# Kernel optimization log

Measured on AMD Instinct MI355X. Metric: run time of the kernel, lower is better.

## Reference

```python
import jax, jax.numpy as jnp
import numpy as np

DIM = 512
CROSS_DIM = 512
NUM_HEADS = 8
DIM_HEAD = 64
INNER = NUM_HEADS * DIM_HEAD  # 512
SCALE = DIM_HEAD ** -0.5


def setup_inputs() -> dict:
    key = jax.random.key(0)
    ks = jax.random.split(key, 7)
    B, S, C = 2, 4096, 4096
    x = jax.random.normal(ks[0], (B, S, DIM), dtype=jnp.float32)
    context = jax.random.normal(ks[1], (B, C, CROSS_DIM), dtype=jnp.float32)
    # nn.Linear weights stored as [out, in]; we apply x @ W.T
    w_q = jax.random.normal(ks[2], (INNER, DIM), dtype=jnp.float32) * (DIM ** -0.5)
    w_k = jax.random.normal(ks[3], (INNER, CROSS_DIM), dtype=jnp.float32) * (CROSS_DIM ** -0.5)
    w_v = jax.random.normal(ks[4], (INNER, CROSS_DIM), dtype=jnp.float32) * (CROSS_DIM ** -0.5)
    w_out = jax.random.normal(ks[5], (DIM, INNER), dtype=jnp.float32) * (INNER ** -0.5)
    b_out = jax.random.normal(ks[6], (DIM,), dtype=jnp.float32) * 0.02
    return {"x": x, "context": context, "w_q": w_q, "w_k": w_k,
            "w_v": w_v, "w_out": w_out, "b_out": b_out}


def reference(x, context, w_q, w_k, w_v, w_out, b_out):
    B, S, _ = x.shape
    _, C, _ = context.shape
    # projections -> [B, H, L, Dh]
    q = (x @ w_q.T).reshape(B, S, NUM_HEADS, DIM_HEAD).transpose(0, 2, 1, 3)
    k = (context @ w_k.T).reshape(B, C, NUM_HEADS, DIM_HEAD).transpose(0, 2, 1, 3)
    v = (context @ w_v.T).reshape(B, C, NUM_HEADS, DIM_HEAD).transpose(0, 2, 1, 3)
    # scores [B, H, S, C]
    scores = jnp.einsum('bhsd,bhcd->bhsc', q, k) * SCALE
    attn = jax.nn.softmax(scores, axis=-1)
    out = jnp.einsum('bhsc,bhcd->bhsd', attn, v)  # [B,H,S,Dh]
    out = out.transpose(0, 2, 1, 3).reshape(B, S, INNER)
    return out @ w_out.T + b_out
```

## Files before the change

### kernel.cpp

```cpp
#include <hip/hip_runtime.h>

typedef __bf16 bf16;
typedef __bf16 bf16x2 __attribute__((ext_vector_type(2)));
typedef __bf16 bf16x4 __attribute__((ext_vector_type(4)));
typedef __bf16 bf16x8 __attribute__((ext_vector_type(8)));
typedef float  f32x4  __attribute__((ext_vector_type(4)));
typedef float  f32x16 __attribute__((ext_vector_type(16)));
typedef unsigned int uint4v __attribute__((ext_vector_type(4)));

#define MFMA16(a,b,c) __builtin_amdgcn_mfma_f32_16x16x32_bf16(a,b,c,0,0,0)
#define MFMA32(a,b,c) __builtin_amdgcn_mfma_f32_32x32x16_bf16(a,b,c,0,0,0)

#if __has_builtin(__builtin_amdgcn_exp2f)
#define EXP2(x) __builtin_amdgcn_exp2f(x)
#else
#define EXP2(x) exp2f(x)
#endif

__device__ __forceinline__ void gl16(const bf16* __restrict__ g, bf16* l)
{
#if __has_builtin(__builtin_amdgcn_global_load_lds)
    __builtin_amdgcn_global_load_lds(
        (const __attribute__((address_space(1))) void*)g,
        (__attribute__((address_space(3))) void*)l, 16, 0, 0);
#else
    const int ln = __builtin_amdgcn_mbcnt_hi(~0u, __builtin_amdgcn_mbcnt_lo(~0u, 0));
    *(bf16x8*)((bf16*)l + ln * 8) = *(const bf16x8*)g;
#endif
}

__device__ __forceinline__ bf16x8 ld8_f32_to_bf16(const float* __restrict__ p)
{
    f32x4 a = *(const f32x4*)p;
    f32x4 b = *(const f32x4*)(p + 4);
    bf16x8 o;
#pragma unroll
    for (int j = 0; j < 4; j++) { o[j] = (bf16)a[j]; o[4 + j] = (bf16)b[j]; }
    return o;
}

__device__ __forceinline__ float max3f(float a, float b, float c)
{
    return fmaxf(fmaxf(a, b), c);
}

__device__ __forceinline__ float rmax16(const f32x16& s)
{
    const float a0 = max3f(s[0],  s[1],  s[2]);
    const float a1 = max3f(s[3],  s[4],  s[5]);
    const float a2 = max3f(s[6],  s[7],  s[8]);
    const float a3 = max3f(s[9],  s[10], s[11]);
    const float a4 = max3f(s[12], s[13], s[14]);
    return fmaxf(max3f(a0, a1, a2), max3f(a3, a4, s[15]));
}

__global__ __launch_bounds__(256) void cvt6(
    const float* __restrict__ x,  const float* __restrict__ ctx,
    const float* __restrict__ wq, const float* __restrict__ wk,
    const float* __restrict__ wv, const float* __restrict__ wout,
    bf16* __restrict__ xb, bf16* __restrict__ cb, bf16* __restrict__ wqb,
    bf16* __restrict__ wkb, bf16* __restrict__ wvb, bf16* __restrict__ wob)
{
    const int bid = blockIdx.x;
    const float* s; bf16* d; int base;
    if      (bid < 2048) { s = x;    d = xb;  base = 0;    }
    else if (bid < 4096) { s = ctx;  d = cb;  base = 2048; }
    else if (bid < 4224) { s = wq;   d = wqb; base = 4096; }
    else if (bid < 4352) { s = wk;   d = wkb; base = 4224; }
    else if (bid < 4480) { s = wv;   d = wvb; base = 4352; }
    else                 { s = wout; d = wob; base = 4480; }
    const int i = ((bid - base) * 256 + threadIdx.x) * 8;
    *(bf16x8*)&d[i] = ld8_f32_to_bf16(s + i);
}

__global__ __launch_bounds__(256, 3) void mm_qkv(
    const bf16* __restrict__ xb, const bf16* __restrict__ cb,
    const bf16* __restrict__ wqb, const bf16* __restrict__ wkb,
    const bf16* __restrict__ wvb,
    bf16* __restrict__ Qb, bf16* __restrict__ Kb, bf16* __restrict__ Vtb)
{
    __shared__ bf16 Al[128 * 32];
    __shared__ bf16 Wl[128 * 32];

    const int L  = blockIdx.x + 4 * (blockIdx.y + 64 * blockIdx.z);
    const int L2 = (L & 7) * 96 + (L >> 3);
    const int bx = L2 & 3;
    const int by = (L2 >> 2) & 63;
    const int z  = L2 >> 8;

    const bf16* A; const bf16* W; bf16* out; int mode;
    if (z == 0)      { A = xb; W = wqb; out = Qb;  mode = 0; }
    else if (z == 1) { A = cb; W = wkb; out = Kb;  mode = 0; }
    else             { A = cb; W = wvb; out = Vtb; mode = 1; }

    const int tid  = threadIdx.x;
    const int lane = tid & 63;
    const int w    = tid >> 6;
    const int wr   = w >> 1, wc = w & 1;
    const int q    = lane >> 4, m0 = lane & 15;

    f32x4 acc[4][4];
#pragma unroll
    for (int i = 0; i < 4; i++)
#pragma unroll
        for (int j = 0; j < 4; j++)
#pragma unroll
            for (int r = 0; r < 4; r++) acc[i][j][r] = 0.f;

    const bf16* Ab = A + (size_t)(by * 128) * 512;
    const bf16* Wb = W + (size_t)(bx * 128) * 512;
    const int sr = w * 16 + (lane >> 2);
    const int sc = (lane & 3) * 8;

    for (int k0 = 0; k0 < 512; k0 += 32) {
        gl16(Ab + (size_t)sr * 512 + k0 + sc,        &Al[(w * 16) * 32]);
        gl16(Ab + (size_t)(sr + 64) * 512 + k0 + sc, &Al[(64 + w * 16) * 32]);
        gl16(Wb + (size_t)sr * 512 + k0 + sc,        &Wl[(w * 16) * 32]);
        gl16(Wb + (size_t)(sr + 64) * 512 + k0 + sc, &Wl[(64 + w * 16) * 32]);
        __syncthreads();

        bf16x8 af[4], wf[4];
#pragma unroll
        for (int mt = 0; mt < 4; mt++)
            af[mt] = *(const bf16x8*)&Al[(wr * 64 + mt * 16 + m0) * 32 + q * 8];
#pragma unroll
        for (int nt = 0; nt < 4; nt++)
            wf[nt] = *(const bf16x8*)&Wl[(wc * 64 + nt * 16 + m0) * 32 + q * 8];
#pragma unroll
        for (int mt = 0; mt < 4; mt++)
#pragma unroll
            for (int nt = 0; nt < 4; nt++)
                acc[mt][nt] = MFMA16(af[mt], wf[nt], acc[mt][nt]);
        __syncthreads();
    }

#pragma unroll
    for (int nt = 0; nt < 4; nt++) {
        const int col = bx * 128 + wc * 64 + nt * 16 + m0;
#pragma unroll
        for (int mt = 0; mt < 4; mt++) {
            const int row0 = by * 128 + wr * 64 + mt * 16 + q * 4;
            if (mode == 0) {
#pragma unroll
                for (int r = 0; r < 4; r++)
                    out[(size_t)(row0 + r) * 512 + col] = (bf16)acc[mt][nt][r];
            } else {
                const int bb = row0 >> 12, c = row0 & 4095;
                const int hh = col >> 6,  d = col & 63;
                bf16x4 o4;
#pragma unroll
                for (int r = 0; r < 4; r++) o4[r] = (bf16)acc[mt][nt][r];
                *(bf16x4*)&out[(size_t)((bb * 8 + hh) * 64 + d) * 4096 + c] = o4;
            }
        }
    }
}

__global__ __launch_bounds__(256, 3) void mm_oproj(
    const bf16* __restrict__ Ob, const bf16* __restrict__ wob,
    const float* __restrict__ bout, float* __restrict__ out)
{
    __shared__ bf16 Al[128 * 32];
    __shared__ bf16 Wl[128 * 32];

    const int L  = blockIdx.x + 4 * blockIdx.y;
    const int L2 = (L & 7) * 32 + (L >> 3);
    const int bx = L2 & 3;
    const int by = L2 >> 2;

    const int tid  = threadIdx.x;
    const int lane = tid & 63;
    const int w    = tid >> 6;
    const int wr   = w >> 1, wc = w & 1;
    const int q    = lane >> 4, m0 = lane & 15;

    f32x4 acc[4][4];
#pragma unroll
    for (int i = 0; i < 4; i++)
#pragma unroll
        for (int j = 0; j < 4; j++)
#pragma unroll
            for (int r = 0; r < 4; r++) acc[i][j][r] = 0.f;

    const bf16* Ab = Ob  + (size_t)(by * 128) * 512;
    const bf16* Wb = wob + (size_t)(bx * 128) * 512;
    const int sr = w * 16 + (lane >> 2);
    const int sc = (lane & 3) * 8;

    for (int k0 = 0; k0 < 512; k0 += 32) {
        gl16(Ab + (size_t)sr * 512 + k0 + sc,        &Al[(w * 16) * 32]);
        gl16(Ab + (size_t)(sr + 64) * 512 + k0 + sc, &Al[(64 + w * 16) * 32]);
        gl16(Wb + (size_t)sr * 512 + k0 + sc,        &Wl[(w * 16) * 32]);
        gl16(Wb + (size_t)(sr + 64) * 512 + k0 + sc, &Wl[(64 + w * 16) * 32]);
        __syncthreads();

        bf16x8 af[4], wf[4];
#pragma unroll
        for (int mt = 0; mt < 4; mt++)
            af[mt] = *(const bf16x8*)&Al[(wr * 64 + mt * 16 + m0) * 32 + q * 8];
#pragma unroll
        for (int nt = 0; nt < 4; nt++)
            wf[nt] = *(const bf16x8*)&Wl[(wc * 64 + nt * 16 + m0) * 32 + q * 8];
#pragma unroll
        for (int mt = 0; mt < 4; mt++)
#pragma unroll
            for (int nt = 0; nt < 4; nt++)
                acc[mt][nt] = MFMA16(af[mt], wf[nt], acc[mt][nt]);
        __syncthreads();
    }

#pragma unroll
    for (int nt = 0; nt < 4; nt++) {
        const int col = bx * 128 + wc * 64 + nt * 16 + m0;
        const float bv = bout[col];
#pragma unroll
        for (int mt = 0; mt < 4; mt++) {
#pragma unroll
            for (int r = 0; r < 4; r++) {
                const int row = by * 128 + wr * 64 + mt * 16 + q * 4 + r;
                out[(size_t)row * 512 + col] = acc[mt][nt][r] + bv;
            }
        }
    }
}

__global__ __launch_bounds__(256, 2) void fa_attn(
    const bf16* __restrict__ Qb, const bf16* __restrict__ Kb,
    const bf16* __restrict__ Vtb, bf16* __restrict__ Ob,
    float* __restrict__ Opart, float2* __restrict__ ml, const int nsplit)
{
    __shared__ bf16 Kl[2][64 * 72];
    __shared__ bf16 Vl[2][64 * 72];

    const int tid  = threadIdx.x;
    const int lane = tid & 63;
    const int w    = tid >> 6;
    const int n0   = lane & 31;
    const int hd   = lane >> 5;

    const int nper = 64 * nsplit;
    const int L  = blockIdx.x + 32 * (blockIdx.y + 8 * blockIdx.z);
    const int L2 = (L & 7) * nper + (L >> 3);
    const int qx = L2 & 31;
    const int yz = L2 >> 5;
    const int h0 = yz & 7;
    const int zz = yz >> 3;
    const int b  = (nsplit == 2) ? (zz >> 1) : zz;
    const int ch = (nsplit == 2) ? (zz & 1) : 0;
    const int clen = (nsplit == 2) ? 2048 : 4096;
    const int c0 = ch * clen;
    const int qg = qx * 128 + w * 32;

    const float qsc = 0.125f * 1.44269504089f;
    bf16x8 qf[4];
    const bf16* qp = Qb + (size_t)(b * 4096 + qg + n0) * 512 + h0 * 64 + hd * 8;
#pragma unroll
    for (int ks = 0; ks < 4; ks++) {
        bf16x8 t = *(const bf16x8*)(qp + ks * 16);
#pragma unroll
        for (int j = 0; j < 8; j++) t[j] = (bf16)((float)t[j] * qsc);
        qf[ks] = t;
    }

    f32x16 oc[2];
#pragma unroll
    for (int dt = 0; dt < 2; dt++)
#pragma unroll
        for (int r = 0; r < 16; r++) oc[dt][r] = 0.f;
    float mrun = -1e30f, lrun = 0.f;

    const int srow = tid >> 2;
    const int scol = (tid & 3) * 16;
    const bf16* Kg = Kb  + (size_t)(b * 4096) * 512 + h0 * 64;
    const bf16* Vg = Vtb + (size_t)(b * 8 + h0) * 64 * 4096;

#define STAGE(buf, cb_) do { \
    *(bf16x8*)&Kl[buf][srow * 72 + scol]     = *(const bf16x8*)(Kg + (size_t)((cb_) + srow) * 512 + scol); \
    *(bf16x8*)&Kl[buf][srow * 72 + scol + 8] = *(const bf16x8*)(Kg + (size_t)((cb_) + srow) * 512 + scol + 8); \
    *(bf16x8*)&Vl[buf][srow * 72 + scol]     = *(const bf16x8*)(Vg + (size_t)srow * 4096 + (cb_) + scol); \
    *(bf16x8*)&Vl[buf][srow * 72 + scol + 8] = *(const bf16x8*)(Vg + (size_t)srow * 4096 + (cb_) + scol + 8); \
} while (0)

    STAGE(0, c0);
    int cur = 0;

    for (int cb = c0; cb < c0 + clen; cb += 64) {
        __syncthreads();
        if (cb + 64 < c0 + clen) STAGE(cur ^ 1, cb + 64);

        const bf16* Kc = &Kl[cur][0];
        const bf16* Vc = &Vl[cur][0];

        f32x16 st[2];
        __builtin_amdgcn_s_setprio(1);
#pragma unroll
        for (int ct = 0; ct < 2; ct++) {
#pragma unroll
            for (int r = 0; r < 16; r++) st[ct][r] = 0.f;
#pragma unroll
            for (int ks = 0; ks < 4; ks++) {
                bf16x8 kf = *(const bf16x8*)&Kc[(ct * 32 + n0) * 72 + ks * 16 + hd * 8];
                st[ct] = MFMA32(kf, qf[ks], st[ct]);
            }
        }
        __builtin_amdgcn_s_setprio(0);

        float mx = fmaxf(rmax16(st[0]), rmax16(st[1]));
        mx = fmaxf(mx, __shfl_xor(mx, 32));

        if (__any(mx > mrun + 8.f)) {
            const float mnew = fmaxf(mrun, mx);
            const float al = EXP2(mrun - mnew);
            mrun = mnew;
            lrun *= al;
#pragma unroll
            for (int dt = 0; dt < 2; dt++)
#pragma unroll
                for (int r = 0; r < 16; r++) oc[dt][r] *= al;
        }

        unsigned int pd[2][4][2];
        float rs4[4];
#pragma unroll
        for (int g = 0; g < 4; g++) rs4[g] = 0.f;
#pragma unroll
        for (int ct = 0; ct < 2; ct++)
#pragma unroll
            for (int g = 0; g < 4; g++)
#pragma unroll
                for (int t = 0; t < 2; t++) {
                    const float e0 = EXP2(st[ct][4 * g + 2 * t]     - mrun);
                    const float e1 = EXP2(st[ct][4 * g + 2 * t + 1] - mrun);
                    rs4[g] += e0 + e1;
                    bf16x2 pr; pr[0] = (bf16)e0; pr[1] = (bf16)e1;
                    pd[ct][g][t] = __builtin_bit_cast(unsigned int, pr);
                }
        float rs = (rs4[0] + rs4[1]) + (rs4[2] + rs4[3]);
        rs += __shfl_xor(rs, 32);
        lrun += rs;

        __builtin_amdgcn_s_setprio(1);
#pragma unroll
        for (int ks = 0; ks < 4; ks++) {
            const int ct = ks >> 1;
            const int g0 = 2 * (ks & 1), g1 = g0 + 1;
            const unsigned int own0  = hd ? pd[ct][g1][0] : pd[ct][g0][0];
            const unsigned int own1  = hd ? pd[ct][g1][1] : pd[ct][g0][1];
            const unsigned int send0 = hd ? pd[ct][g0][0] : pd[ct][g1][0];
            const unsigned int send1 = hd ? pd[ct][g0][1] : pd[ct][g1][1];
            const unsigned int r0 = (unsigned int)__shfl_xor((int)send0, 32);
            const unsigned int r1 = (unsigned int)__shfl_xor((int)send1, 32);
            uint4v u;
            u[0] = hd ? r0 : own0;
            u[1] = hd ? r1 : own1;
            u[2] = hd ? own0 : r0;
            u[3] = hd ? own1 : r1;
            const bf16x8 pf = __builtin_bit_cast(bf16x8, u);
#pragma unroll
            for (int dt = 0; dt < 2; dt++) {
                bf16x8 vf = *(const bf16x8*)&Vc[(dt * 32 + n0) * 72 + ks * 16 + hd * 8];
                oc[dt] = MFMA32(vf, pf, oc[dt]);
            }
        }
        __builtin_amdgcn_s_setprio(0);
        cur ^= 1;
    }
#undef STAGE

    if (nsplit == 1) {
        const float rli = 1.0f / lrun;
        bf16* ob = Ob + (size_t)(b * 4096 + qg + n0) * 512 + h0 * 64;
#pragma unroll
        for (int dt = 0; dt < 2; dt++)
#pragma unroll
            for (int rq = 0; rq < 4; rq++) {
                bf16x4 o4;
#pragma unroll
                for (int i = 0; i < 4; i++) o4[i] = (bf16)(oc[dt][4 * rq + i] * rli);
                *(bf16x4*)&ob[dt * 32 + rq * 8 + hd * 4] = o4;
            }
    } else {
        float* Op = Opart + ((size_t)(ch * 2 + b) * 4096 + qg + n0) * 512 + h0 * 64;
#pragma unroll
        for (int dt = 0; dt < 2; dt++)
#pragma unroll
            for (int rq = 0; rq < 4; rq++) {
                f32x4 o4;
#pragma unroll
                for (int i = 0; i < 4; i++) o4[i] = oc[dt][4 * rq + i];
                *(f32x4*)&Op[dt * 32 + rq * 8 + hd * 4] = o4;
            }
        if (hd == 0)
            ml[((size_t)(ch * 2 + b) * 8 + h0) * 4096 + qg + n0] = make_float2(mrun, lrun);
    }
}

__global__ __launch_bounds__(256) void fa_merge(
    const float* __restrict__ Opart, const float2* __restrict__ ml,
    bf16* __restrict__ Ob)
{
    const int e   = blockIdx.x * 256 + threadIdx.x;
    const int row = e >> 7;
    const int c4  = (e & 127) * 4;
    const int b   = row >> 12, sr = row & 4095, h = c4 >> 6;

    const float2 u = ml[((size_t)(0 + b) * 8 + h) * 4096 + sr];
    const float2 v = ml[((size_t)(2 + b) * 8 + h) * 4096 + sr];
    const float m  = fmaxf(u.x, v.x);
    const float w1 = EXP2(u.x - m), w2 = EXP2(v.x - m);
    const float rL = 1.0f / (u.y * w1 + v.y * w2);

    const f32x4 o1 = *(const f32x4*)&Opart[((size_t)(0 + b) * 4096 + sr) * 512 + c4];
    const f32x4 o2 = *(const f32x4*)&Opart[((size_t)(2 + b) * 4096 + sr) * 512 + c4];
    bf16x4 o;
#pragma unroll
    for (int i = 0; i < 4; i++) o[i] = (bf16)((o1[i] * w1 + o2[i] * w2) * rL);
    *(bf16x4*)&Ob[(size_t)row * 512 + c4] = o;
}

__global__ void ws_sig11(float* out) { if (threadIdx.x == 0) out[0] = 777.0f; }

extern "C" void kernel_launch(void* const* d_in, const int* in_sizes, int n_in,
                              void* d_out, int out_size, void* d_ws, size_t ws_size,
                              hipStream_t stream)
{
    const float* x    = (const float*)d_in[0];
    const float* ctx  = (const float*)d_in[1];
    const float* wq   = (const float*)d_in[2];
    const float* wk   = (const float*)d_in[3];
    const float* wv   = (const float*)d_in[4];
    const float* wout = (const float*)d_in[5];
    const float* bout = (const float*)d_in[6];
    float* out = (float*)d_out;

    char* ws = (char*)d_ws;
    const size_t MB = 1024 * 1024;
    const size_t SZ = (size_t)8192 * 512 * sizeof(bf16);
    if (ws_size < 66 * MB) {
        ws_sig11<<<dim3(1), dim3(64), 0, stream>>>(out);
        return;
    }

    bf16* Qb  = (bf16*)(ws);
    bf16* Kb  = (bf16*)(ws + SZ);
    bf16* Vtb = (bf16*)(ws + 2 * SZ);
    bf16* Ob  = (bf16*)(ws + 3 * SZ);

    bf16* xb  = (bf16*)(ws + 32 * MB);
    bf16* cbf = (bf16*)(ws + 40 * MB);
    bf16* wqb = (bf16*)(ws + 48 * MB);
    bf16* wkb = (bf16*)(ws + 48 * MB + 512 * 1024);
    bf16* wvb = (bf16*)(ws + 49 * MB);
    float*  Opart = (float*)(ws + 32 * MB);
    float2* mlp   = (float2*)(ws + 64 * MB);
    bf16*   wob   = (bf16*)(ws + 65 * MB);

    cvt6    <<<dim3(4608), dim3(256), 0, stream>>>(x, ctx, wq, wk, wv, wout,
                                                   xb, cbf, wqb, wkb, wvb, wob);
    mm_qkv  <<<dim3(4, 64, 3), dim3(256), 0, stream>>>(xb, cbf, wqb, wkb, wvb, Qb, Kb, Vtb);
    fa_attn <<<dim3(32, 8, 4), dim3(256), 0, stream>>>(Qb, Kb, Vtb, Ob, Opart, mlp, 2);
    fa_merge<<<dim3(4096), dim3(256), 0, stream>>>(Opart, mlp, Ob);
    mm_oproj<<<dim3(4, 64, 1), dim3(256), 0, stream>>>(Ob, wob, bout, out);
}
```

Measured before the change: 223.8 us.

## Fuse split-KV merge into output projection and vectorize GEMM epilogues

Removes the separate fa_merge kernel and performs the two-split softmax recombination inside mm_oproj. Each block precomputes per-row/head merge weights in LDS, then reads both fp32 partial outputs, combines them and writes bf16 into the A tile on the fly. The output tile is narrowed to 128x64 to increase block count, and MFMA operands are swapped so epilogues write contiguous vector stores in both the Q/K projection and the output projection. The cost is that each oproj block now rereads fp32 partials (redundantly across 8 column blocks) instead of bf16, and the A tile is loaded synchronously through registers, losing the direct global-to-LDS load.

Result: slower. 253.6 us (+13.3%).

```diff
diff --git a/kernel.cpp b/kernel.cpp
--- a/kernel.cpp
+++ b/kernel.cpp
@@ -126,25 +126,42 @@
 #pragma unroll
         for (int nt = 0; nt < 4; nt++)
             wf[nt] = *(const bf16x8*)&Wl[(wc * 64 + nt * 16 + m0) * 32 + q * 8];
-#pragma unroll
-        for (int mt = 0; mt < 4; mt++)
-#pragma unroll
-            for (int nt = 0; nt < 4; nt++)
-                acc[mt][nt] = MFMA16(af[mt], wf[nt], acc[mt][nt]);
+        if (mode == 0) {
+#pragma unroll
+            for (int mt = 0; mt < 4; mt++)
+#pragma unroll
+                for (int nt = 0; nt < 4; nt++)
+                    acc[mt][nt] = MFMA16(wf[nt], af[mt], acc[mt][nt]);
+        } else {
+#pragma unroll
+            for (int mt = 0; mt < 4; mt++)
+#pragma unroll
+                for (int nt = 0; nt < 4; nt++)
+                    acc[mt][nt] = MFMA16(af[mt], wf[nt], acc[mt][nt]);
+        }
         __syncthreads();
     }
 
-#pragma unroll
-    for (int nt = 0; nt < 4; nt++) {
-        const int col = bx * 128 + wc * 64 + nt * 16 + m0;
+    if (mode == 0) {
 #pragma unroll
         for (int mt = 0; mt < 4; mt++) {
-            const int row0 = by * 128 + wr * 64 + mt * 16 + q * 4;
-            if (mode == 0) {
-#pragma unroll
-                for (int r = 0; r < 4; r++)
-                    out[(size_t)(row0 + r) * 512 + col] = (bf16)acc[mt][nt][r];
-            } else {
+            const int row = by * 128 + wr * 64 + mt * 16 + m0;
+#pragma unroll
+            for (int nt = 0; nt < 4; nt++) {
+                const int colb = bx * 128 + wc * 64 + nt * 16 + q * 4;
+                bf16x4 o4;
+#pragma unroll
+                for (int i = 0; i < 4; i++) o4[i] = (bf16)acc[mt][nt][i];
+                *(bf16x4*)&out[(size_t)row * 512 + colb] = o4;
+            }
+        }
+    } else {
+#pragma unroll
+        for (int nt = 0; nt < 4; nt++) {
+            const int col = bx * 128 + wc * 64 + nt * 16 + m0;
+#pragma unroll
+            for (int mt = 0; mt < 4; mt++) {
+                const int row0 = by * 128 + wr * 64 + mt * 16 + q * 4;
                 const int bb = row0 >> 12, c = row0 & 4095;
                 const int hh = col >> 6,  d = col & 63;
                 bf16x4 o4;
@@ -156,17 +173,19 @@
     }
 }
 
-__global__ __launch_bounds__(256, 3) void mm_oproj(
-    const bf16* __restrict__ Ob, const bf16* __restrict__ wob,
+__global__ __launch_bounds__(256, 2) void mm_oproj(
+    const float* __restrict__ Opart, const float2* __restrict__ ml,
+    const bf16* __restrict__ wob,
     const float* __restrict__ bout, float* __restrict__ out)
 {
     __shared__ bf16 Al[128 * 32];
-    __shared__ bf16 Wl[128 * 32];
-
-    const int L  = blockIdx.x + 4 * blockIdx.y;
-    const int L2 = (L & 7) * 32 + (L >> 3);
-    const int bx = L2 & 3;
-    const int by = L2 >> 2;
+    __shared__ bf16 Wl[64 * 32];
+    __shared__ float2 wls[128 * 8];
+
+    const int L  = blockIdx.x + 8 * blockIdx.y;
+    const int L2 = (L & 7) * 64 + (L >> 3);
+    const int bx = L2 & 7;
+    const int by = L2 >> 3;
 
     const int tid  = threadIdx.x;
     const int lane = tid & 63;
@@ -174,52 +193,84 @@
     const int wr   = w >> 1, wc = w & 1;
     const int q    = lane >> 4, m0 = lane & 15;
 
-    f32x4 acc[4][4];
+    for (int e = tid; e < 1024; e += 256) {
+        const int r = e >> 3, h = e & 7;
+        const int gr = by * 128 + r;
+        const int b = gr >> 12, sr4 = gr & 4095;
+        const float2 u = ml[((size_t)(0 + b) * 8 + h) * 4096 + sr4];
+        const float2 v = ml[((size_t)(2 + b) * 8 + h) * 4096 + sr4];
+        const float m  = fmaxf(u.x, v.x);
+        const float w1 = EXP2(u.x - m), w2 = EXP2(v.x - m);
+        const float rL = 1.0f / (u.y * w1 + v.y * w2);
+        wls[e] = make_float2(w1 * rL, w2 * rL);
+    }
+
+    f32x4 acc[4][2];
 #pragma unroll
     for (int i = 0; i < 4; i++)
 #pragma unroll
-        for (int j = 0; j < 4; j++)
+        for (int j = 0; j < 2; j++)
 #pragma unroll
             for (int r = 0; r < 4; r++) acc[i][j][r] = 0.f;
 
-    const bf16* Ab = Ob  + (size_t)(by * 128) * 512;
-    const bf16* Wb = wob + (size_t)(bx * 128) * 512;
+    const bf16* Wb = wob + (size_t)(bx * 64) * 512;
     const int sr = w * 16 + (lane >> 2);
     const int sc = (lane & 3) * 8;
+    const int r1 = tid >> 2;
+    const float* o1base = Opart + (size_t)(by * 128) * 512;
+    const float* o2base = o1base + (size_t)8192 * 512;
+
+    __syncthreads();
 
     for (int k0 = 0; k0 < 512; k0 += 32) {
-        gl16(Ab + (size_t)sr * 512 + k0 + sc,        &Al[(w * 16) * 32]);
-        gl16(Ab + (size_t)(sr + 64) * 512 + k0 + sc, &Al[(64 + w * 16) * 32]);
-        gl16(Wb + (size_t)sr * 512 + k0 + sc,        &Wl[(w * 16) * 32]);
-        gl16(Wb + (size_t)(sr + 64) * 512 + k0 + sc, &Wl[(64 + w * 16) * 32]);
+        const int h = k0 >> 6;
+#pragma unroll
+        for (int half = 0; half < 2; half++) {
+            const int r = r1 + half * 64;
+            const float* o1p = o1base + (size_t)r * 512 + k0 + sc;
+            const float* o2p = o2base + (size_t)r * 512 + k0 + sc;
+            const f32x4 a0 = *(const f32x4*)o1p;
+            const f32x4 a1 = *(const f32x4*)(o1p + 4);
+            const f32x4 b0 = *(const f32x4*)o2p;
+            const f32x4 b1 = *(const f32x4*)(o2p + 4);
+            const float2 ww = wls[r * 8 + h];
+            bf16x8 m8;
+#pragma unroll
+            for (int j = 0; j < 4; j++) {
+                m8[j]     = (bf16)(a0[j] * ww.x + b0[j] * ww.y);
+                m8[4 + j] = (bf16)(a1[j] * ww.x + b1[j] * ww.y);
+            }
+            *(bf16x8*)&Al[r * 32 + sc] = m8;
+        }
+        gl16(Wb + (size_t)sr * 512 + k0 + sc, &Wl[(w * 16) * 32]);
         __syncthreads();
 
-        bf16x8 af[4], wf[4];
+        bf16x8 af[4], wf[2];
 #pragma unroll
         for (int mt = 0; mt < 4; mt++)
             af[mt] = *(const bf16x8*)&Al[(wr * 64 + mt * 16 + m0) * 32 + q * 8];
 #pragma unroll
-        for (int nt = 0; nt < 4; nt++)
-            wf[nt] = *(const bf16x8*)&Wl[(wc * 64 + nt * 16 + m0) * 32 + q * 8];
+        for (int nt = 0; nt < 2; nt++)
+            wf[nt] = *(const bf16x8*)&Wl[(wc * 32 + nt * 16 + m0) * 32 + q * 8];
 #pragma unroll
         for (int mt = 0; mt < 4; mt++)
 #pragma unroll
-            for (int nt = 0; nt < 4; nt++)
-                acc[mt][nt] = MFMA16(af[mt], wf[nt], acc[mt][nt]);
+            for (int nt = 0; nt < 2; nt++)
+                acc[mt][nt] = MFMA16(wf[nt], af[mt], acc[mt][nt]);
         __syncthreads();
     }
 
 #pragma unroll
-    for (int nt = 0; nt < 4; nt++) {
-        const int col = bx * 128 + wc * 64 + nt * 16 + m0;
-        const float bv = bout[col];
-#pragma unroll
-        for (int mt = 0; mt < 4; mt++) {
-#pragma unroll
-            for (int r = 0; r < 4; r++) {
-                const int row = by * 128 + wr * 64 + mt * 16 + q * 4 + r;
-                out[(size_t)row * 512 + col] = acc[mt][nt][r] + bv;
-            }
+    for (int mt = 0; mt < 4; mt++) {
+        const int row = by * 128 + wr * 64 + mt * 16 + m0;
+#pragma unroll
+        for (int nt = 0; nt < 2; nt++) {
+            const int colb = bx * 64 + wc * 32 + nt * 16 + q * 4;
+            const f32x4 bv4 = *(const f32x4*)&bout[colb];
+            f32x4 o;
+#pragma unroll
+            for (int i = 0; i < 4; i++) o[i] = acc[mt][nt][i] + bv4[i];
+            *(f32x4*)&out[(size_t)row * 512 + colb] = o;
         }
     }
 }
@@ -395,29 +446,6 @@
     }
 }
 
-__global__ __launch_bounds__(256) void fa_merge(
-    const float* __restrict__ Opart, const float2* __restrict__ ml,
-    bf16* __restrict__ Ob)
-{
-    const int e   = blockIdx.x * 256 + threadIdx.x;
-    const int row = e >> 7;
-    const int c4  = (e & 127) * 4;
-    const int b   = row >> 12, sr = row & 4095, h = c4 >> 6;
-
-    const float2 u = ml[((size_t)(0 + b) * 8 + h) * 4096 + sr];
-    const float2 v = ml[((size_t)(2 + b) * 8 + h) * 4096 + sr];
-    const float m  = fmaxf(u.x, v.x);
-    const float w1 = EXP2(u.x - m), w2 = EXP2(v.x - m);
-    const float rL = 1.0f / (u.y * w1 + v.y * w2);
-
-    const f32x4 o1 = *(const f32x4*)&Opart[((size_t)(0 + b) * 4096 + sr) * 512 + c4];
-    const f32x4 o2 = *(const f32x4*)&Opart[((size_t)(2 + b) * 4096 + sr) * 512 + c4];
-    bf16x4 o;
-#pragma unroll
-    for (int i = 0; i < 4; i++) o[i] = (bf16)((o1[i] * w1 + o2[i] * w2) * rL);
-    *(bf16x4*)&Ob[(size_t)row * 512 + c4] = o;
-}
-
 __global__ void ws_sig11(float* out) { if (threadIdx.x == 0) out[0] = 777.0f; }
 
 extern "C" void kernel_launch(void* const* d_in, const int* in_sizes, int n_in,
@@ -459,6 +487,5 @@
                                                    xb, cbf, wqb, wkb, wvb, wob);
     mm_qkv  <<<dim3(4, 64, 3), dim3(256), 0, stream>>>(xb, cbf, wqb, wkb, wvb, Qb, Kb, Vtb);
     fa_attn <<<dim3(32, 8, 4), dim3(256), 0, stream>>>(Qb, Kb, Vtb, Ob, Opart, mlp, 2);
-    fa_merge<<<dim3(4096), dim3(256), 0, stream>>>(Opart, mlp, Ob);
-    mm_oproj<<<dim3(4, 64, 1), dim3(256), 0, stream>>>(Ob, wob, bout, out);
-}
+    mm_oproj<<<dim3(8, 64), dim3(256), 0, stream>>>(Opart, mlp, wob, bout, out);
+}
```
